# Kernel optimization log

Measured on AMD Instinct MI355X. Metric: run time of the kernel, lower is better.

## Reference

```python
import jax, jax.numpy as jnp
import numpy as np


def _gauss_kernel():
    # Matches create_gaussian_kernel(sigma=0.25, n_sigmas_per_side=4, n_dims=2)
    sigma = 0.25
    n_sig = 4
    t = np.linspace(-sigma * n_sig / 2, sigma * n_sig / 2, int(sigma * n_sig + 1))  # 2 taps
    g = np.exp(-0.5 * (t / sigma) ** 2)
    k2d = g[:, None] * g[None, :]
    return (k2d / k2d.sum()).astype(np.float32)  # (2, 2), each entry 0.25


def setup_inputs() -> dict:
    key = jax.random.key(0)
    x = jax.random.normal(key, (32, 512, 512, 3), dtype=jnp.float32)  # NHWC
    kernel = jnp.asarray(_gauss_kernel())  # (2, 2) blur kernel (constant in the layer)
    return {"x": x, "kernel": kernel}


def reference(x, kernel):
    # Original: per-channel tf.nn.conv2d with the same 2x2 kernel, stride 2, SAME pad,
    # then restack channels. Equivalent fused form: depthwise strided convolution.
    c = x.shape[-1]
    # HWIO depthwise kernel: (kh, kw, in_per_group=1, out=c), same weights per channel
    k = jnp.tile(kernel[:, :, None, None], (1, 1, 1, c))
    out = jax.lax.conv_general_dilated(
        x, k,
        window_strides=(2, 2),
        padding='SAME',
        dimension_numbers=('NHWC', 'HWIO', 'NHWC'),
        feature_group_count=c,
    )  # (B, ceil(H/2), ceil(W/2), C)
    return out
```

## Files before the change

### kernel.cpp

```cpp
#include <hip/hip_runtime.h>


#define BATCH 32
#define H 512
#define W 512
#define C 3
#define OH (H / 2)
#define OW (W / 2)
#define ROWF (W * C)
#define OROWF (OW * C)

__global__ __launch_bounds__(256) void blur_ds_kernel(
    const float* __restrict__ x, const float* __restrict__ kern,
    float* __restrict__ out) {
  __shared__ float lds[2 * ROWF];

  const int blk = blockIdx.x;
  const int t = threadIdx.x;

  const float k00 = kern[0];
  const float k01 = kern[1];
  const float k10 = kern[2];
  const float k11 = kern[3];

  const int b = blk >> 8;
  const int oh = blk & 255;

  const float* src = x + (size_t)(b * H + 2 * oh) * ROWF;

  const float4* s4 = (const float4*)src;
  float4* l4 = (float4*)lds;
#pragma unroll
  for (int i = 0; i < 3; ++i) {
    l4[t + i * 256] = s4[t + i * 256];
  }
  __syncthreads();

  float* orow = out + (size_t)blk * OROWF;

#pragma unroll
  for (int i = 0; i < 3; ++i) {
    const int f = t + i * 256;
    const int ow = f / 3;
    const int c = f - 3 * ow;
    const int g = 6 * ow + c;
    const float v = k00 * lds[g] + k01 * lds[g + 3] + k10 * lds[ROWF + g] +
                    k11 * lds[ROWF + g + 3];
    orow[f] = v;
  }
}

extern "C" void kernel_launch(void* const* d_in, const int* in_sizes, int n_in,
                              void* d_out, int out_size, void* d_ws,
                              size_t ws_size, hipStream_t stream) {
  const float* x = (const float*)d_in[0];
  const float* kern = (const float*)d_in[1];
  float* out = (float*)d_out;

  const int nblocks = BATCH * OH;
  blur_ds_kernel<<<nblocks, 256, 0, stream>>>(x, kern, out);
}
```

Measured before the change: 23.91 us.

## Replace LDS staging with per-thread register blocking and float4 stores

Each thread now loads 24 contiguous floats from each of the two input rows straight into registers and computes 4 output pixels (12 floats). These are written back as three float4 stores. This removes the shared-memory staging, the barrier and the scalar output stores, and it quadruples the work per thread with fewer blocks. The cost is strided per-lane global loads (96-byte stride across lanes), which may coalesce worse than the old contiguous float4 loads, plus higher register pressure.

Result: no change. 24.13 us (+0.9%).

```diff
diff --git a/kernel.cpp b/kernel.cpp
--- a/kernel.cpp
+++ b/kernel.cpp
@@ -1,53 +1,53 @@
 #include <hip/hip_runtime.h>
 
 
-#define BATCH 32
-#define H 512
-#define W 512
-#define C 3
-#define OH (H / 2)
-#define OW (W / 2)
-#define ROWF (W * C)
-#define OROWF (OW * C)
+#define ROWF 1536
+#define NBLOCKS 2048
 
 __global__ __launch_bounds__(256) void blur_ds_kernel(
     const float* __restrict__ x, const float* __restrict__ kern,
     float* __restrict__ out) {
-  __shared__ float lds[2 * ROWF];
-
-  const int blk = blockIdx.x;
-  const int t = threadIdx.x;
+  const int g = blockIdx.x * 256 + threadIdx.x;
+  const int r = g >> 6;
+  const int lane = g & 63;
 
   const float k00 = kern[0];
   const float k01 = kern[1];
   const float k10 = kern[2];
   const float k11 = kern[3];
 
-  const int b = blk >> 8;
-  const int oh = blk & 255;
+  const float4* s0 = (const float4*)(x + (size_t)r * (2 * ROWF) + lane * 24);
+  const float4* s1 = s0 + (ROWF / 4);
 
-  const float* src = x + (size_t)(b * H + 2 * oh) * ROWF;
+  float af[24], bf[24];
+#pragma unroll
+  for (int j = 0; j < 6; ++j) {
+    const float4 v = s0[j];
+    af[4 * j + 0] = v.x; af[4 * j + 1] = v.y;
+    af[4 * j + 2] = v.z; af[4 * j + 3] = v.w;
+  }
+#pragma unroll
+  for (int j = 0; j < 6; ++j) {
+    const float4 v = s1[j];
+    bf[4 * j + 0] = v.x; bf[4 * j + 1] = v.y;
+    bf[4 * j + 2] = v.z; bf[4 * j + 3] = v.w;
+  }
 
-  const float4* s4 = (const float4*)src;
-  float4* l4 = (float4*)lds;
+  float of[12];
 #pragma unroll
-  for (int i = 0; i < 3; ++i) {
-    l4[t + i * 256] = s4[t + i * 256];
+  for (int p = 0; p < 4; ++p) {
+#pragma unroll
+    for (int c = 0; c < 3; ++c) {
+      const int gi = 6 * p + c;
+      of[3 * p + c] = k00 * af[gi] + k01 * af[gi + 3] +
+                      k10 * bf[gi] + k11 * bf[gi + 3];
+    }
   }
-  __syncthreads();
 
-  float* orow = out + (size_t)blk * OROWF;
-
-#pragma unroll
-  for (int i = 0; i < 3; ++i) {
-    const int f = t + i * 256;
-    const int ow = f / 3;
-    const int c = f - 3 * ow;
-    const int g = 6 * ow + c;
-    const float v = k00 * lds[g] + k01 * lds[g + 3] + k10 * lds[ROWF + g] +
-                    k11 * lds[ROWF + g + 3];
-    orow[f] = v;
-  }
+  float4* o4 = (float4*)(out + (size_t)g * 12);
+  o4[0] = make_float4(of[0], of[1], of[2], of[3]);
+  o4[1] = make_float4(of[4], of[5], of[6], of[7]);
+  o4[2] = make_float4(of[8], of[9], of[10], of[11]);
 }
 
 extern "C" void kernel_launch(void* const* d_in, const int* in_sizes, int n_in,
@@ -57,6 +57,5 @@
   const float* kern = (const float*)d_in[1];
   float* out = (float*)d_out;
 
-  const int nblocks = BATCH * OH;
-  blur_ds_kernel<<<nblocks, 256, 0, stream>>>(x, kern, out);
+  blur_ds_kernel<<<NBLOCKS, 256, 0, stream>>>(x, kern, out);
 }
```
